# Performance work log

Hardware: AMD Instinct MI355X
Metric: run time of the kernel (lower is better)

The kernel has to match this reference:

```python
import jax, jax.numpy as jnp
import numpy as np

EPS = 1e-10   # eps added inside cumprod, as in _compute_weights
FAR = 1e10    # last delta, as in forward()
NEAR_D, FAR_D = 2.0, 6.0  # typical NeRF near/far bounds for depth sampling

N_RAYS, N_PTS = 65536, 128


def setup_inputs() -> dict:
    key = jax.random.key(0)
    k1, k2, k3 = jax.random.split(key, 3)
    # densities are non-negative (raw sigma output after relu/softplus)
    density = jax.random.uniform(k1, (N_RAYS, N_PTS), dtype=jnp.float32) * 2.0
    feature = jax.random.uniform(k2, (N_RAYS, N_PTS, 3), dtype=jnp.float32)
    # monotonically increasing sample depths along each ray in [NEAR_D, FAR_D]
    depth_values = jnp.sort(
        jax.random.uniform(k3, (N_RAYS, N_PTS), dtype=jnp.float32,
                           minval=NEAR_D, maxval=FAR_D), axis=-1)
    return {"density": density, "feature": feature, "depth_values": depth_values}


def reference(density, feature, depth_values):
    # deltas: diff of sample depths, last delta = 1e10  -> [N, P]
    deltas = jnp.concatenate(
        [depth_values[..., 1:] - depth_values[..., :-1],
         jnp.full_like(depth_values[..., :1], FAR)], axis=-1)
    alpha = 1.0 - jnp.exp(-deltas * density)                      # [N, P]
    # transmittance: cumprod(1-alpha+eps) rolled right with T[...,0]=1
    Tinc = jnp.cumprod(1.0 - alpha + EPS, axis=-1)                # [N, P]
    T = jnp.concatenate([jnp.ones_like(Tinc[..., :1]), Tinc[..., :-1]], axis=-1)
    weights = T * alpha                                           # [N, P]
    # weighted feature (rgb) and depth aggregation over samples
    rgb = jnp.einsum('np,npc->nc', weights, feature)              # [N, 3]
    depth = jnp.einsum('np,npc->nc', weights,
                       jnp.broadcast_to(depth_values[..., None], feature.shape))  # [N, 3]
    return rgb, depth
```

## Files before the change

### kernel.cpp

```cpp
#include <hip/hip_runtime.h>

#define N_PTS 128
#define EPS_F 1e-10f
#define FAR_F 1e10f

typedef float f4 __attribute__((ext_vector_type(4)));

template<int CTRL, int ROW_MASK>
__device__ __forceinline__ float dpp_mov(float src, float old) {
    union { float f; int i; } s, o, r;
    s.f = src; o.f = old;
    r.i = __builtin_amdgcn_update_dpp(o.i, s.i, CTRL, ROW_MASK, 0xF, false);
    return r.f;
}

__device__ __forceinline__ float half32_reduce_add(float x) {
    x += dpp_mov<0x111, 0xF>(x, 0.0f);
    x += dpp_mov<0x112, 0xF>(x, 0.0f);
    x += dpp_mov<0x114, 0xF>(x, 0.0f);
    x += dpp_mov<0x118, 0xF>(x, 0.0f);
    x += dpp_mov<0x142, 0xA>(x, 0.0f);
    return x;
}

__global__ __launch_bounds__(256) void volrend_kernel(
        const float* __restrict__ density,
        const float* __restrict__ feature,
        const float* __restrict__ depth,
        float* __restrict__ out, int n_rays) {
    const int lane = threadIdx.x & 63;
    const int sub  = lane & 31;
    const int h    = lane >> 5;
    const int ray  = blockIdx.x * 8 + (threadIdx.x >> 6) * 2 + h;
    if (ray >= n_rays) return;

    const size_t doff = (size_t)ray * N_PTS + (sub << 2);
    const f4 dns = __builtin_nontemporal_load((const f4*)(density + doff));
    const f4 zz  = __builtin_nontemporal_load((const f4*)(depth   + doff));
    const f4* fp = (const f4*)(feature + (size_t)ray * (N_PTS * 3) + sub * 12);
    const f4 fa = __builtin_nontemporal_load(fp + 0);
    const f4 fb = __builtin_nontemporal_load(fp + 1);
    const f4 fc = __builtin_nontemporal_load(fp + 2);

    float nz = dpp_mov<0x130, 0xF>(zz.x, 0.0f);
    float d0 = zz.y - zz.x;
    float d1 = zz.z - zz.y;
    float d2 = zz.w - zz.z;
    float d3 = (sub == 31) ? FAR_F : (nz - zz.w);

    float e0 = __expf(-d0 * dns.x);
    float e1 = __expf(-d1 * dns.y);
    float e2 = __expf(-d2 * dns.z);
    float e3 = __expf(-d3 * dns.w);
    float a0 = 1.0f - e0, a1 = 1.0f - e1, a2 = 1.0f - e2, a3 = 1.0f - e3;
    float f0 = e0 + EPS_F, f1 = e1 + EPS_F, f2 = e2 + EPS_F, f3 = e3 + EPS_F;

    float f01  = f0 * f1;
    float f012 = f01 * f2;
    float p    = f012 * f3;
    p *= dpp_mov<0x111, 0xF>(p, 1.0f);
    p *= dpp_mov<0x112, 0xF>(p, 1.0f);
    p *= dpp_mov<0x114, 0xF>(p, 1.0f);
    p *= dpp_mov<0x118, 0xF>(p, 1.0f);
    p *= dpp_mov<0x142, 0xA>(p, 1.0f);
    float Ts = dpp_mov<0x138, 0xF>(p, 1.0f);
    if (sub == 0) Ts = 1.0f;

    float w0 = Ts * a0;
    float T1 = Ts * f0;   float w1 = T1 * a1;
    float T2 = Ts * f01;  float w2 = T2 * a2;
    float T3 = Ts * f012; float w3 = T3 * a3;

    float rx = half32_reduce_add(w0 * fa.x + w1 * fa.w + w2 * fb.z + w3 * fc.y);
    float ry = half32_reduce_add(w0 * fa.y + w1 * fb.x + w2 * fb.w + w3 * fc.z);
    float rz = half32_reduce_add(w0 * fa.z + w1 * fb.y + w2 * fc.x + w3 * fc.w);
    float dd = half32_reduce_add(w0 * zz.x + w1 * zz.y + w2 * zz.z + w3 * zz.w);

    if (sub == 31) {
        float* o  = out + (size_t)ray * 3;
        o[0] = rx; o[1] = ry; o[2] = rz;
        float* od = out + (size_t)n_rays * 3 + (size_t)ray * 3;
        od[0] = dd; od[1] = dd; od[2] = dd;
    }
}

extern "C" void kernel_launch(void* const* d_in, const int* in_sizes, int n_in,
                              void* d_out, int out_size, void* d_ws, size_t ws_size,
                              hipStream_t stream) {
    const float* density = (const float*)d_in[0];
    const float* feature = (const float*)d_in[1];
    const float* depth   = (const float*)d_in[2];
    float* out = (float*)d_out;
    const int n_rays = in_sizes[0] / N_PTS;
    const int blocks = (n_rays + 7) / 8;
    volrend_kernel<<<blocks, 256, 0, stream>>>(density, feature, depth, out, n_rays);
}
```

Measured before the change: 180.4 us.

## Batch four ray pairs per wave with all loads issued before compute

Each wavefront now handles eight rays (four pairs). All global loads for the four pairs are issued up front, and a scheduling barrier keeps them ahead of the compute, so more memory requests are in flight per wave. The grid shrinks fourfold, and a launch bound hint caps occupancy while register use grows. Output stores become nontemporal. A tail path handles ray counts that are not a multiple of eight.

```diff
diff --git a/kernel.cpp b/kernel.cpp
--- a/kernel.cpp
+++ b/kernel.cpp
@@ -23,35 +23,33 @@
     return x;
 }
 
-__global__ __launch_bounds__(256) void volrend_kernel(
-        const float* __restrict__ density,
-        const float* __restrict__ feature,
-        const float* __restrict__ depth,
-        float* __restrict__ out, int n_rays) {
-    const int lane = threadIdx.x & 63;
-    const int sub  = lane & 31;
-    const int h    = lane >> 5;
-    const int ray  = blockIdx.x * 8 + (threadIdx.x >> 6) * 2 + h;
-    if (ray >= n_rays) return;
+struct Pair { f4 d, z, fa, fb, fc; };
 
+__device__ __forceinline__ void load_pair(
+        Pair& P, const float* __restrict__ density,
+        const float* __restrict__ feature, const float* __restrict__ depth,
+        int ray, int sub) {
     const size_t doff = (size_t)ray * N_PTS + (sub << 2);
-    const f4 dns = __builtin_nontemporal_load((const f4*)(density + doff));
-    const f4 zz  = __builtin_nontemporal_load((const f4*)(depth   + doff));
+    P.d  = __builtin_nontemporal_load((const f4*)(density + doff));
+    P.z  = __builtin_nontemporal_load((const f4*)(depth   + doff));
     const f4* fp = (const f4*)(feature + (size_t)ray * (N_PTS * 3) + sub * 12);
-    const f4 fa = __builtin_nontemporal_load(fp + 0);
-    const f4 fb = __builtin_nontemporal_load(fp + 1);
-    const f4 fc = __builtin_nontemporal_load(fp + 2);
+    P.fa = __builtin_nontemporal_load(fp + 0);
+    P.fb = __builtin_nontemporal_load(fp + 1);
+    P.fc = __builtin_nontemporal_load(fp + 2);
+}
 
-    float nz = dpp_mov<0x130, 0xF>(zz.x, 0.0f);
-    float d0 = zz.y - zz.x;
-    float d1 = zz.z - zz.y;
-    float d2 = zz.w - zz.z;
-    float d3 = (sub == 31) ? FAR_F : (nz - zz.w);
+__device__ __forceinline__ void process_pair(
+        const Pair& P, int sub, int ray, int n_rays, float* __restrict__ out) {
+    float nz = dpp_mov<0x130, 0xF>(P.z.x, 0.0f);
+    float d0 = P.z.y - P.z.x;
+    float d1 = P.z.z - P.z.y;
+    float d2 = P.z.w - P.z.z;
+    float d3 = (sub == 31) ? FAR_F : (nz - P.z.w);
 
-    float e0 = __expf(-d0 * dns.x);
-    float e1 = __expf(-d1 * dns.y);
-    float e2 = __expf(-d2 * dns.z);
-    float e3 = __expf(-d3 * dns.w);
+    float e0 = __expf(-d0 * P.d.x);
+    float e1 = __expf(-d1 * P.d.y);
+    float e2 = __expf(-d2 * P.d.z);
+    float e3 = __expf(-d3 * P.d.w);
     float a0 = 1.0f - e0, a1 = 1.0f - e1, a2 = 1.0f - e2, a3 = 1.0f - e3;
     float f0 = e0 + EPS_F, f1 = e1 + EPS_F, f2 = e2 + EPS_F, f3 = e3 + EPS_F;
 
@@ -71,16 +69,54 @@
     float T2 = Ts * f01;  float w2 = T2 * a2;
     float T3 = Ts * f012; float w3 = T3 * a3;
 
-    float rx = half32_reduce_add(w0 * fa.x + w1 * fa.w + w2 * fb.z + w3 * fc.y);
-    float ry = half32_reduce_add(w0 * fa.y + w1 * fb.x + w2 * fb.w + w3 * fc.z);
-    float rz = half32_reduce_add(w0 * fa.z + w1 * fb.y + w2 * fc.x + w3 * fc.w);
-    float dd = half32_reduce_add(w0 * zz.x + w1 * zz.y + w2 * zz.z + w3 * zz.w);
+    float rx = half32_reduce_add(w0 * P.fa.x + w1 * P.fa.w + w2 * P.fb.z + w3 * P.fc.y);
+    float ry = half32_reduce_add(w0 * P.fa.y + w1 * P.fb.x + w2 * P.fb.w + w3 * P.fc.z);
+    float rz = half32_reduce_add(w0 * P.fa.z + w1 * P.fb.y + w2 * P.fc.x + w3 * P.fc.w);
+    float dd = half32_reduce_add(w0 * P.z.x  + w1 * P.z.y  + w2 * P.z.z  + w3 * P.z.w);
 
     if (sub == 31) {
         float* o  = out + (size_t)ray * 3;
-        o[0] = rx; o[1] = ry; o[2] = rz;
+        __builtin_nontemporal_store(rx, o + 0);
+        __builtin_nontemporal_store(ry, o + 1);
+        __builtin_nontemporal_store(rz, o + 2);
         float* od = out + (size_t)n_rays * 3 + (size_t)ray * 3;
-        od[0] = dd; od[1] = dd; od[2] = dd;
+        __builtin_nontemporal_store(dd, od + 0);
+        __builtin_nontemporal_store(dd, od + 1);
+        __builtin_nontemporal_store(dd, od + 2);
+    }
+}
+
+__global__ __launch_bounds__(256, 2) void volrend_kernel(
+        const float* __restrict__ density,
+        const float* __restrict__ feature,
+        const float* __restrict__ depth,
+        float* __restrict__ out, int n_rays) {
+    const int lane = threadIdx.x & 63;
+    const int sub  = lane & 31;
+    const int h    = lane >> 5;
+    const int gw   = blockIdx.x * 4 + (threadIdx.x >> 6);
+    const int base = gw * 8;
+
+    if (base + 8 <= n_rays) {
+        Pair P0, P1, P2, P3;
+        load_pair(P0, density, feature, depth, base + 0 + h, sub);
+        load_pair(P1, density, feature, depth, base + 2 + h, sub);
+        load_pair(P2, density, feature, depth, base + 4 + h, sub);
+        load_pair(P3, density, feature, depth, base + 6 + h, sub);
+        __builtin_amdgcn_sched_barrier(0);
+        process_pair(P0, sub, base + 0 + h, n_rays, out);
+        process_pair(P1, sub, base + 2 + h, n_rays, out);
+        process_pair(P2, sub, base + 4 + h, n_rays, out);
+        process_pair(P3, sub, base + 6 + h, n_rays, out);
+    } else {
+        for (int pi = 0; pi < 4; ++pi) {
+            const int ray = base + 2 * pi + h;
+            if (ray < n_rays) {
+                Pair P;
+                load_pair(P, density, feature, depth, ray, sub);
+                process_pair(P, sub, ray, n_rays, out);
+            }
+        }
     }
 }
 
@@ -92,6 +128,6 @@
     const float* depth   = (const float*)d_in[2];
     float* out = (float*)d_out;
     const int n_rays = in_sizes[0] / N_PTS;
-    const int blocks = (n_rays + 7) / 8;
+    const int blocks = (n_rays + 31) / 32;
     volrend_kernel<<<blocks, 256, 0, stream>>>(density, feature, depth, out, n_rays);
 }
```

After: 187.5 us. +3.9%, slower.
